# Kernel optimization log

Measured on AMD Instinct MI355X. Metric: run time of the kernel, lower is better.

Reference implementation:

```python
import jax, jax.numpy as jnp
import numpy as np

NL, D, DI, N, R, K = 32, 256, 512, 16, 16, 4   # layers, d_model, d_inner, d_state, dt_rank, d_conv
V, FF, BATCH, L = 4096, 1024, 32, 256


def _mamba_layer(x, p):
    # x: (B, L, D). One pre-norm Mamba block with residual: x + mamba(LN(x)).
    ln_w, ln_b, in_w, cw, cb, xp_w, dtw, dtb, A_log, Dskip, out_w = p
    mu = x.mean(-1, keepdims=True)
    var = ((x - mu) ** 2).mean(-1, keepdims=True)
    h = (x - mu) / jnp.sqrt(var + 1e-5) * ln_w + ln_b
    xz = jnp.einsum('bld,ed->ble', h, in_w)            # (B, L, 2*DI)
    xm, z = jnp.split(xz, 2, axis=-1)
    seq = xm.shape[1]
    # causal depthwise conv1d, kernel K, then SiLU
    xpad = jnp.pad(xm, ((0, 0), (K - 1, 0), (0, 0)))
    xc = sum(xpad[:, k:k + seq] * cw[:, k] for k in range(K)) + cb
    xc = jax.nn.silu(xc)
    dbc = jnp.einsum('ble,fe->blf', xc, xp_w)          # (B, L, R+2N)
    dt, Bm, Cm = jnp.split(dbc, [R, R + N], axis=-1)
    dt = jax.nn.softplus(jnp.einsum('blr,er->ble', dt, dtw) + dtb)  # (B, L, DI)
    A = -jnp.exp(A_log)                                # (DI, N)

    def step(hs, inp):
        dt_t, B_t, C_t, x_t = inp                      # (B,DI),(B,N),(B,N),(B,DI)
        dA = jnp.exp(dt_t[..., None] * A)              # (B, DI, N)
        hs = hs * dA + (dt_t * x_t)[..., None] * B_t[:, None, :]
        return hs, jnp.einsum('ben,bn->be', hs, C_t)

    h0 = jnp.zeros((xc.shape[0], DI, N), xc.dtype)
    _, ys = jax.lax.scan(step, h0, (dt.swapaxes(0, 1), Bm.swapaxes(0, 1), Cm.swapaxes(0, 1), xc.swapaxes(0, 1)))
    y = ys.swapaxes(0, 1) + xc * Dskip
    y = y * jax.nn.silu(z)
    return x + jnp.einsum('ble,de->bld', y, out_w)


def _stack_forward(x, params):
    return jax.lax.scan(lambda c, p: (jax.checkpoint(_mamba_layer)(c, p), None), x, params)[0]


def setup_inputs() -> dict:
    key = jax.random.key(0)
    ks = jax.random.split(key, 12)
    rn = lambda k, shape, s=0.02: jax.random.normal(k, shape, jnp.float32) * s
    return {
        'token_ids': jax.random.randint(ks[0], (BATCH, L), 0, V),
        'emb': rn(ks[1], (V, D)),
        'ln_w': jnp.ones((NL, D)), 'ln_b': jnp.zeros((NL, D)),
        'in_proj_w': rn(ks[2], (NL, 2 * DI, D)),
        'conv_w': rn(ks[3], (NL, DI, K), 0.1), 'conv_b': jnp.zeros((NL, DI)),
        'x_proj_w': rn(ks[4], (NL, R + 2 * N, DI)),
        'dt_w': rn(ks[5], (NL, DI, R), 0.1),
        'dt_b': jnp.full((NL, DI), float(np.log(np.expm1(0.01))), jnp.float32),
        'A_log': jnp.broadcast_to(jnp.log(jnp.arange(1, N + 1, dtype=jnp.float32)), (NL, DI, N)) + 0.0,
        'Dskip': jnp.ones((NL, DI)),
        'out_proj_w': rn(ks[6], (NL, D, DI)),
        'W1': rn(ks[7], (FF, D)), 'b1': jnp.zeros((FF,)),
        'W2': rn(ks[8], (V, FF)), 'b2': jnp.zeros((V,)),
    }


def reference(token_ids, emb, ln_w, ln_b, in_proj_w, conv_w, conv_b, x_proj_w, dt_w, dt_b, A_log, Dskip, out_proj_w, W1, b1, W2, b2):
    x = emb[token_ids]                                  # (B, L, D)
    params = (ln_w, ln_b, in_proj_w, conv_w, conv_b, x_proj_w, dt_w, dt_b, A_log, Dskip, out_proj_w)
    x = _stack_forward(x, params)                       # 32 stacked Mamba blocks
    h = jax.nn.relu(x @ W1.T + b1)
    return h @ W2.T + b2                                # (B, L, V) logits
```

## Files before the change

### kernel.cpp

```cpp
#include <hip/hip_runtime.h>
#include <hip/hip_bf16.h>
#include <cstdint>
#include <cstddef>


typedef __bf16 v8bf __attribute__((ext_vector_type(8)));
typedef float  v4f  __attribute__((ext_vector_type(4)));

__device__ __forceinline__ void async_copy16(const void* g, void* l) {
  __builtin_amdgcn_global_load_lds((const __attribute__((address_space(1))) void*)g,
                                   (__attribute__((address_space(3))) void*)l, 16, 0, 0);
}

__device__ __forceinline__ float bf(__bf16 v) { return (float)v; }

constexpr size_t OFF_WIN  = 0;
constexpr size_t OFF_WXP  = 16777216;
constexpr size_t OFF_WOUT = 18350080;
constexpr size_t OFF_WW1  = 26738688;
constexpr size_t OFF_WW2  = 27262976;
constexpr size_t OFF_X    = 35651584;
constexpr size_t OFF_H    = 44040192;
constexpr size_t OFF_XZ   = 48234496;
constexpr size_t OFF_DBC  = 73400320;
constexpr size_t OFF_PART = 83361792;
constexpr size_t OFF_PROD = 91750400;

__global__ __launch_bounds__(256)
void f2b_multi(const float* __restrict__ s0, const float* __restrict__ s1,
               const float* __restrict__ s2, const float* __restrict__ s3,
               const float* __restrict__ s4, char* __restrict__ ws) {
  size_t i = (size_t)blockIdx.x * 256 + threadIdx.x;
  if (i < 8388608) { ((__bf16*)(ws + OFF_WIN))[i] = (__bf16)s0[i]; return; }
  i -= 8388608;
  if (i < 786432)  { ((__bf16*)(ws + OFF_WXP))[i] = (__bf16)s1[i]; return; }
  i -= 786432;
  if (i < 4194304) { ((__bf16*)(ws + OFF_WOUT))[i] = (__bf16)s2[i]; return; }
  i -= 4194304;
  if (i < 262144)  { ((__bf16*)(ws + OFF_WW1))[i] = (__bf16)s3[i]; return; }
  i -= 262144;
  ((__bf16*)(ws + OFF_WW2))[i] = (__bf16)s4[i];
}

__global__ __launch_bounds__(256) void f2b_k(const float* __restrict__ X,
                                             __bf16* __restrict__ O) {
  size_t i = (size_t)blockIdx.x * 256 + threadIdx.x;
  O[i] = (__bf16)X[i];
}

__global__ __launch_bounds__(256)
void embed_ln_k(const int* __restrict__ tok, const float* __restrict__ emb,
                const float* __restrict__ w, const float* __restrict__ b,
                float* __restrict__ X, __bf16* __restrict__ H) {
  int row = blockIdx.x;
  int t   = threadIdx.x;
  float v = emb[(size_t)tok[row] * 256 + t];
  X[(size_t)row * 256 + t] = v;
  float s = v, q = v * v;
  #pragma unroll
  for (int o = 32; o > 0; o >>= 1) { s += __shfl_xor(s, o); q += __shfl_xor(q, o); }
  __shared__ float ss[4], qq[4];
  int wv = t >> 6;
  if ((t & 63) == 0) { ss[wv] = s; qq[wv] = q; }
  __syncthreads();
  s = ss[0] + ss[1] + ss[2] + ss[3];
  q = qq[0] + qq[1] + qq[2] + qq[3];
  float mu  = s * (1.f / 256.f);
  float var = q * (1.f / 256.f) - mu * mu;
  float r   = rsqrtf(var + 1e-5f);
  H[(size_t)row * 256 + t] = (__bf16)((v - mu) * r * w[t] + b[t]);
}

template <int EPI>
__global__ __launch_bounds__(256, 2)
void gemm_bt(const __bf16* __restrict__ A, const __bf16* __restrict__ W,
             void* outp, const float* __restrict__ bias, int M, int N, int K) {
  __shared__ __align__(16) __bf16 sA[128 * 32];
  __shared__ __align__(16) __bf16 sB[128 * 32];
  const int tid  = threadIdx.x;
  const int bm0  = blockIdx.y << 7;
  const int bn0  = blockIdx.x << 7;
  const int lane = tid & 63;
  const int wv   = tid >> 6;
  const int wm   = (wv >> 1) << 6;
  const int wn   = (wv & 1) << 6;
  const int lr   = lane & 15;
  const int lk   = lane >> 4;

  v4f acc[4][4] = {};

  const int r0 = tid >> 2;
  const int c0 = (tid & 3) << 3;
  const int wbase = (tid & ~63) << 3;

  const __bf16* gA0 = A + (size_t)(bm0 + r0) * K + c0;
  const __bf16* gA1 = A + (size_t)(bm0 + 64 + r0) * K + c0;
  const __bf16* gB0 = W + (size_t)(bn0 + r0) * K + c0;
  const __bf16* gB1 = W + (size_t)(bn0 + 64 + r0) * K + c0;

  for (int kk = 0; kk < K; kk += 32) {
    async_copy16(gA0 + kk, sA + wbase);
    async_copy16(gA1 + kk, sA + 2048 + wbase);
    async_copy16(gB0 + kk, sB + wbase);
    async_copy16(gB1 + kk, sB + 2048 + wbase);
    __syncthreads();
    v8bf af[4], bfr[4];
    #pragma unroll
    for (int i = 0; i < 4; ++i)
      af[i] = *(const v8bf*)(sA + ((wm + i * 16 + lr) << 5) + (lk << 3));
    #pragma unroll
    for (int j = 0; j < 4; ++j)
      bfr[j] = *(const v8bf*)(sB + ((wn + j * 16 + lr) << 5) + (lk << 3));
    #pragma unroll
    for (int i = 0; i < 4; ++i)
      #pragma unroll
      for (int j = 0; j < 4; ++j)
        acc[i][j] = __builtin_amdgcn_mfma_f32_16x16x32_bf16(af[i], bfr[j], acc[i][j], 0, 0, 0);
    __syncthreads();
  }

  #pragma unroll
  for (int i = 0; i < 4; ++i) {
    #pragma unroll
    for (int j = 0; j < 4; ++j) {
      int gc = bn0 + wn + j * 16 + lr;
      #pragma unroll
      for (int v = 0; v < 4; ++v) {
        int gr = bm0 + wm + i * 16 + (lk << 2) + v;
        float val = acc[i][j][v];
        size_t idx = (size_t)gr * N + gc;
        if (EPI == 0) {
          ((__bf16*)outp)[idx] = (__bf16)val;
        } else if (EPI == 1) {
          val += bias[gc]; val = fmaxf(val, 0.f);
          ((__bf16*)outp)[idx] = (__bf16)val;
        } else {
          ((float*)outp)[idx] = val + bias[gc];
        }
      }
    }
  }
}

__global__ __launch_bounds__(512, 2)
void convscan1_k(const __bf16* __restrict__ XZ,
                 const float* __restrict__ cw, const float* __restrict__ cb,
                 const __bf16* __restrict__ Wxp,
                 const float* __restrict__ dtw, const float* __restrict__ dtb,
                 const float* __restrict__ Alog,
                 float* __restrict__ DBC,
                 float* __restrict__ PART, float* __restrict__ PROD) {
  __shared__ __align__(16) __bf16 sXC[32 * 512];
  __shared__ __align__(16) float  sDBC[32 * 48];
  const int tid = threadIdx.x;
  const int c   = blockIdx.x >> 5;
  const int b   = blockIdx.x & 31;
  const int bl0 = b * 256 + c * 32;

  {
    const int r  = tid >> 4;
    const int ec = tid & 15;
    #pragma unroll
    for (int j = 0; j < 4; ++j) {
      const int e = (ec << 3) + (j << 7);
      v4f cw4[8];
      #pragma unroll
      for (int jj = 0; jj < 8; ++jj) cw4[jj] = *(const v4f*)(cw + (size_t)(e + jj) * 4);
      float a[8];
      #pragma unroll
      for (int jj = 0; jj < 8; ++jj) a[jj] = cb[e + jj];
      #pragma unroll
      for (int k = 0; k < 4; ++k) {
        if (c > 0 || r + k >= 3) {
          const v8bf xv = *(const v8bf*)(XZ + (size_t)(bl0 + r + k - 3) * 1024 + e);
          #pragma unroll
          for (int jj = 0; jj < 8; ++jj) a[jj] += bf(xv[jj]) * cw4[jj][k];
        }
      }
      v8bf outv;
      #pragma unroll
      for (int jj = 0; jj < 8; ++jj) {
        float s = a[jj] / (1.f + __expf(-a[jj]));
        outv[jj] = (__bf16)s;
      }
      const int cbk = (e >> 3) ^ (r & 7);
      *(v8bf*)(sXC + r * 512 + (cbk << 3)) = outv;
    }
  }
  __syncthreads();

  if (tid < 192) {
    const int w = tid >> 6, lane = tid & 63, lr = lane & 15, lk = lane >> 4;
    v4f acc[2] = {};
    for (int kk = 0; kk < 512; kk += 32) {
      const v8bf bfr = *(const v8bf*)(Wxp + (size_t)(w * 16 + lr) * 512 + kk + (lk << 3));
      #pragma unroll
      for (int i = 0; i < 2; ++i) {
        const int row = i * 16 + lr;
        const int cbk = (((kk >> 3) + lk) ^ (row & 7));
        const v8bf af = *(const v8bf*)(sXC + row * 512 + (cbk << 3));
        acc[i] = __builtin_amdgcn_mfma_f32_16x16x32_bf16(af, bfr, acc[i], 0, 0, 0);
      }
    }
    const int gc = w * 16 + lr;
    #pragma unroll
    for (int i = 0; i < 2; ++i)
      #pragma unroll
      for (int v = 0; v < 4; ++v)
        sDBC[(i * 16 + (lk << 2) + v) * 48 + gc] = acc[i][v];
  }
  __syncthreads();

  if (tid < 384)
    *(v4f*)(DBC + (size_t)bl0 * 48 + tid * 4) = *(const v4f*)(sDBC + tid * 4);

  if (c < 7) {
    const int e = tid;
    float Arow2[16], Wdt[16];
    #pragma unroll
    for (int n = 0; n < 16; ++n) {
      Arow2[n] = -1.4426950408889634f * __expf(Alog[(size_t)e * 16 + n]);
      Wdt[n]   = dtw[(size_t)e * 16 + n];
    }
    const float bias = dtb[e];
    float part[16], prod[16];
    #pragma unroll
    for (int n = 0; n < 16; ++n) { part[n] = 0.f; prod[n] = 1.f; }
    for (int tt = 0; tt < 32; ++tt) {
      const v4f* dp = (const v4f*)(sDBC + tt * 48);
      v4f d0 = dp[0], d1 = dp[1], d2 = dp[2], d3 = dp[3];
      v4f bv0 = dp[4], bv1 = dp[5], bv2 = dp[6], bv3 = dp[7];
      float dtv = bias;
      #pragma unroll
      for (int r = 0; r < 4; ++r)
        dtv += d0[r] * Wdt[r] + d1[r] * Wdt[r + 4] + d2[r] * Wdt[r + 8] + d3[r] * Wdt[r + 12];
      dtv = (dtv > 20.f) ? dtv : log1pf(__expf(dtv));
      const float x = bf(sXC[tt * 512 + (((e >> 3) ^ (tt & 7)) << 3) + (e & 7)]);
      const float dtx = dtv * x;
      float Bv[16];
      #pragma unroll
      for (int r = 0; r < 4; ++r) { Bv[r] = bv0[r]; Bv[r+4] = bv1[r]; Bv[r+8] = bv2[r]; Bv[r+12] = bv3[r]; }
      #pragma unroll
      for (int n = 0; n < 16; ++n) {
        const float dA = exp2f(dtv * Arow2[n]);
        part[n] = part[n] * dA + dtx * Bv[n];
        prod[n] *= dA;
      }
    }
    const size_t o = (((size_t)c * 32 + b) * 512 + e) * 16;
    #pragma unroll
    for (int rq = 0; rq < 4; ++rq) {
      v4f p, q;
      #pragma unroll
      for (int v = 0; v < 4; ++v) { p[v] = part[rq * 4 + v]; q[v] = prod[rq * 4 + v]; }
      *(v4f*)(PART + o + rq * 4) = p;
      *(v4f*)(PROD + o + rq * 4) = q;
    }
  }
}

__global__ __launch_bounds__(512, 2)
void scan2out_k(const __bf16* __restrict__ XZ,
                const float* __restrict__ cw, const float* __restrict__ cb,
                const float* __restrict__ DBC,
                const float* __restrict__ dtw, const float* __restrict__ dtb,
                const float* __restrict__ Alog, const float* __restrict__ Dskip,
                const float* __restrict__ PART, const float* __restrict__ PROD,
                const __bf16* __restrict__ Wout,
                const float* __restrict__ lnw, const float* __restrict__ lnb,
                float* __restrict__ X, __bf16* __restrict__ H) {
  __shared__ __align__(16) __bf16 sY[32 * 520];
  __shared__ __align__(16) __bf16 sB[256 * 32];
  __shared__ float sSum[4][32], sSq[4][32];
  const int tid = threadIdx.x;
  const int c   = blockIdx.x >> 5;
  const int b   = blockIdx.x & 31;
  const int bl0 = b * 256 + c * 32;
  const int e   = tid;

  float Arow2[16], Wdt[16];
  #pragma unroll
  for (int n = 0; n < 16; ++n) {
    Arow2[n] = -1.4426950408889634f * __expf(Alog[(size_t)e * 16 + n]);
    Wdt[n]   = dtw[(size_t)e * 16 + n];
  }
  const float bias = dtb[e];
  const float Dsk  = Dskip[e];
  const v4f   cwv  = *(const v4f*)(cw + (size_t)e * 4);
  const float cbe  = cb[e];

  float h[16];
  #pragma unroll
  for (int n = 0; n < 16; ++n) h[n] = 0.f;
  for (int cc = 0; cc < c; ++cc) {
    const size_t o = (((size_t)cc * 32 + b) * 512 + e) * 16;
    #pragma unroll
    for (int rq = 0; rq < 4; ++rq) {
      const v4f p = *(const v4f*)(PART + o + rq * 4);
      const v4f q = *(const v4f*)(PROD + o + rq * 4);
      #pragma unroll
      for (int v = 0; v < 4; ++v) h[rq * 4 + v] = q[v] * h[rq * 4 + v] + p[v];
    }
  }

  float w0 = 0.f, w1 = 0.f, w2 = 0.f;
  if (c > 0) {
    w0 = bf(XZ[(size_t)(bl0 - 3) * 1024 + e]);
    w1 = bf(XZ[(size_t)(bl0 - 2) * 1024 + e]);
    w2 = bf(XZ[(size_t)(bl0 - 1) * 1024 + e]);
  }

  #pragma unroll 2
  for (int tt = 0; tt < 32; ++tt) {
    const float xt = bf(XZ[(size_t)(bl0 + tt) * 1024 + e]);
    float a = cbe + w0 * cwv[0] + w1 * cwv[1] + w2 * cwv[2] + xt * cwv[3];
    const float x = a / (1.f + __expf(-a));
    w0 = w1; w1 = w2; w2 = xt;
    const float* dpf = DBC + (size_t)(bl0 + tt) * 48;
    const v4f* dp = (const v4f*)dpf;
    v4f d0 = dp[0], d1 = dp[1], d2 = dp[2], d3 = dp[3];
    v4f bv0 = dp[4], bv1 = dp[5], bv2 = dp[6], bv3 = dp[7];
    v4f cv0 = dp[8], cv1 = dp[9], cv2 = dp[10], cv3 = dp[11];
    float dtv = bias;
    #pragma unroll
    for (int r = 0; r < 4; ++r)
      dtv += d0[r] * Wdt[r] + d1[r] * Wdt[r + 4] + d2[r] * Wdt[r + 8] + d3[r] * Wdt[r + 12];
    dtv = (dtv > 20.f) ? dtv : log1pf(__expf(dtv));
    const float dtx = dtv * x;
    float Bv[16], Cv[16];
    #pragma unroll
    for (int r = 0; r < 4; ++r) {
      Bv[r] = bv0[r]; Bv[r+4] = bv1[r]; Bv[r+8] = bv2[r]; Bv[r+12] = bv3[r];
      Cv[r] = cv0[r]; Cv[r+4] = cv1[r]; Cv[r+8] = cv2[r]; Cv[r+12] = cv3[r];
    }
    float y = 0.f;
    #pragma unroll
    for (int n = 0; n < 16; ++n) {
      const float dA = exp2f(dtv * Arow2[n]);
      h[n] = h[n] * dA + dtx * Bv[n];
      y += h[n] * Cv[n];
    }
    const float z  = bf(XZ[(size_t)(bl0 + tt) * 1024 + 512 + e]);
    const float sg = z / (1.f + __expf(-z));
    sY[tt * 520 + e] = (__bf16)((y + x * Dsk) * sg);
  }
  __syncthreads();

  const int w = tid >> 6, lane = tid & 63, lr = lane & 15, lk = lane >> 4;
  const int wm = (w & 1) << 4;
  const int wn = (w >> 1) << 6;
  v4f acc[4] = {};
  for (int kk = 0; kk < 512; kk += 32) {
    async_copy16(Wout + (size_t)(tid >> 2) * 512 + ((tid & 3) << 3) + kk,
                 sB + ((tid & ~63) << 3));
    async_copy16(Wout + (size_t)(128 + (tid >> 2)) * 512 + ((tid & 3) << 3) + kk,
                 sB + 4096 + ((tid & ~63) << 3));
    __syncthreads();
    const v8bf af = *(const v8bf*)(sY + (wm + lr) * 520 + kk + (lk << 3));
    #pragma unroll
    for (int j = 0; j < 4; ++j) {
      const v8bf bfr = *(const v8bf*)(sB + ((wn + j * 16 + lr) << 5) + (lk << 3));
      acc[j] = __builtin_amdgcn_mfma_f32_16x16x32_bf16(af, bfr, acc[j], 0, 0, 0);
    }
    __syncthreads();
  }

  float s2[4], q2[4];
  #pragma unroll
  for (int v = 0; v < 4; ++v) {
    const int gr = bl0 + wm + (lk << 2) + v;
    float s = 0.f, q = 0.f;
    #pragma unroll
    for (int j = 0; j < 4; ++j) {
      const int gc = wn + j * 16 + lr;
      float val = X[(size_t)gr * 256 + gc] + acc[j][v];
      acc[j][v] = val;
      s += val; q += val * val;
    }
    #pragma unroll
    for (int o = 8; o > 0; o >>= 1) { s += __shfl_xor(s, o); q += __shfl_xor(q, o); }
    s2[v] = s; q2[v] = q;
  }
  if (lr == 0) {
    #pragma unroll
    for (int v = 0; v < 4; ++v) {
      const int row = wm + (lk << 2) + v;
      sSum[w >> 1][row] = s2[v];
      sSq[w >> 1][row]  = q2[v];
    }
  }
  __syncthreads();
  #pragma unroll
  for (int v = 0; v < 4; ++v) {
    const int row = wm + (lk << 2) + v;
    const float S = sSum[0][row] + sSum[1][row] + sSum[2][row] + sSum[3][row];
    const float Q = sSq[0][row]  + sSq[1][row]  + sSq[2][row]  + sSq[3][row];
    const float mu  = S * (1.f / 256.f);
    const float var = Q * (1.f / 256.f) - mu * mu;
    const float rinv = rsqrtf(var + 1e-5f);
    const int gr = bl0 + row;
    #pragma unroll
    for (int j = 0; j < 4; ++j) {
      const int gc = wn + j * 16 + lr;
      const float val = acc[j][v];
      X[(size_t)gr * 256 + gc] = val;
      H[(size_t)gr * 256 + gc] = (__bf16)((val - mu) * rinv * lnw[gc] + lnb[gc]);
    }
  }
}

extern "C" void kernel_launch(void* const* d_in, const int* in_sizes, int n_in,
                              void* d_out, int out_size, void* d_ws, size_t ws_size,
                              hipStream_t stream) {
  const int*   tok  = (const int*)d_in[0];
  const float* emb  = (const float*)d_in[1];
  const float* lnw  = (const float*)d_in[2];
  const float* lnb  = (const float*)d_in[3];
  const float* inw  = (const float*)d_in[4];
  const float* cw   = (const float*)d_in[5];
  const float* cb   = (const float*)d_in[6];
  const float* xpw  = (const float*)d_in[7];
  const float* dtw  = (const float*)d_in[8];
  const float* dtb  = (const float*)d_in[9];
  const float* alog = (const float*)d_in[10];
  const float* dsk  = (const float*)d_in[11];
  const float* outw = (const float*)d_in[12];
  const float* W1   = (const float*)d_in[13];
  const float* b1   = (const float*)d_in[14];
  const float* W2   = (const float*)d_in[15];
  const float* b2   = (const float*)d_in[16];

  char* ws = (char*)d_ws;
  __bf16* WIN   = (__bf16*)(ws + OFF_WIN);
  __bf16* WXP   = (__bf16*)(ws + OFF_WXP);
  __bf16* WOUT  = (__bf16*)(ws + OFF_WOUT);
  __bf16* WW1   = (__bf16*)(ws + OFF_WW1);
  __bf16* WW2   = (__bf16*)(ws + OFF_WW2);
  float*  X     = (float*)(ws + OFF_X);
  __bf16* H     = (__bf16*)(ws + OFF_H);
  __bf16* XZ    = (__bf16*)(ws + OFF_XZ);
  float*  DBC   = (float*)(ws + OFF_DBC);
  float*  PART  = (float*)(ws + OFF_PART);
  float*  PROD  = (float*)(ws + OFF_PROD);
  __bf16* XB    = (__bf16*)(ws + OFF_PART);
  __bf16* HH    = (__bf16*)(ws + OFF_PROD);

  f2b_multi<<<69632, 256, 0, stream>>>(inw, xpw, outw, W1, W2, ws);
  embed_ln_k<<<8192, 256, 0, stream>>>(tok, emb, lnw, lnb, X, H);

  for (int l = 0; l < 32; ++l) {
    const __bf16* inw_l  = WIN  + (size_t)l * 1024 * 256;
    const float*  cw_l   = cw   + (size_t)l * 512 * 4;
    const float*  cb_l   = cb   + (size_t)l * 512;
    const __bf16* xpw_l  = WXP  + (size_t)l * 48 * 512;
    const float*  dtw_l  = dtw  + (size_t)l * 512 * 16;
    const float*  dtb_l  = dtb  + (size_t)l * 512;
    const float*  alog_l = alog + (size_t)l * 512 * 16;
    const float*  dsk_l  = dsk  + (size_t)l * 512;
    const __bf16* outw_l = WOUT + (size_t)l * 256 * 512;
    const int lnx = (l + 1 < 32) ? l + 1 : 31;

    gemm_bt<0><<<dim3(8, 64), 256, 0, stream>>>(H, inw_l, XZ, nullptr, 8192, 1024, 256);
    convscan1_k<<<256, 512, 0, stream>>>(XZ, cw_l, cb_l, xpw_l, dtw_l, dtb_l,
                                         alog_l, DBC, PART, PROD);
    scan2out_k<<<256, 512, 0, stream>>>(XZ, cw_l, cb_l, DBC, dtw_l, dtb_l,
                                        alog_l, dsk_l, PART, PROD, outw_l,
                                        lnw + (size_t)lnx * 256,
                                        lnb + (size_t)lnx * 256, X, H);
  }

  f2b_k<<<8192, 256, 0, stream>>>(X, XB);
  gemm_bt<1><<<dim3(8, 64), 256, 0, stream>>>(XB, WW1, HH, b1, 8192, 1024, 256);
  gemm_bt<2><<<dim3(32, 64), 256, 0, stream>>>(HH, WW2, (float*)d_out, b2, 8192, 4096, 1024);
}
```

Before: 4.236 ms.

## Fuse next layer's in_proj GEMM into scan2out epilogue with double-buffered XZ

The next layer's input projection (LayerNorm output times W_in) now runs inside scan2out_k's epilogue, using the normalized rows staged in swizzled LDS, and writes XZ for layer l+1 into a ping-pong buffer. This removes a separate GEMM launch per layer and the round trip of H through global memory. The out_proj GEMM also drops its LDS staging of Wout and reads B fragments straight from global memory, removing two barriers per k-step. In exchange the launch bound falls to one block per CU, only 256 blocks do the in_proj work, and every block rereads the full W_in and Wout from cache.

```diff
diff --git a/kernel.cpp b/kernel.cpp
--- a/kernel.cpp
+++ b/kernel.cpp
@@ -21,10 +21,11 @@
 constexpr size_t OFF_WW2  = 27262976;
 constexpr size_t OFF_X    = 35651584;
 constexpr size_t OFF_H    = 44040192;
-constexpr size_t OFF_XZ   = 48234496;
-constexpr size_t OFF_DBC  = 73400320;
+constexpr size_t OFF_XZA  = 48234496;
+constexpr size_t OFF_XZB  = 65011712;
+constexpr size_t OFF_DBC  = 81788928;
 constexpr size_t OFF_PART = 83361792;
-constexpr size_t OFF_PROD = 91750400;
+constexpr size_t OFF_PROD = 90701824;
 
 __global__ __launch_bounds__(256)
 void f2b_multi(const float* __restrict__ s0, const float* __restrict__ s1,
@@ -259,7 +260,7 @@
   }
 }
 
-__global__ __launch_bounds__(512, 2)
+__global__ __launch_bounds__(512, 1)
 void scan2out_k(const __bf16* __restrict__ XZ,
                 const float* __restrict__ cw, const float* __restrict__ cb,
                 const float* __restrict__ DBC,
@@ -268,10 +269,11 @@
                 const float* __restrict__ PART, const float* __restrict__ PROD,
                 const __bf16* __restrict__ Wout,
                 const float* __restrict__ lnw, const float* __restrict__ lnb,
-                float* __restrict__ X, __bf16* __restrict__ H) {
+                float* __restrict__ X,
+                const __bf16* __restrict__ Wnext, __bf16* __restrict__ XZn) {
   __shared__ __align__(16) __bf16 sY[32 * 520];
-  __shared__ __align__(16) __bf16 sB[256 * 32];
   __shared__ float sSum[4][32], sSq[4][32];
+  __bf16* const sH = sY;
   const int tid = threadIdx.x;
   const int c   = blockIdx.x >> 5;
   const int b   = blockIdx.x & 31;
@@ -351,18 +353,12 @@
   const int wn = (w >> 1) << 6;
   v4f acc[4] = {};
   for (int kk = 0; kk < 512; kk += 32) {
-    async_copy16(Wout + (size_t)(tid >> 2) * 512 + ((tid & 3) << 3) + kk,
-                 sB + ((tid & ~63) << 3));
-    async_copy16(Wout + (size_t)(128 + (tid >> 2)) * 512 + ((tid & 3) << 3) + kk,
-                 sB + 4096 + ((tid & ~63) << 3));
-    __syncthreads();
     const v8bf af = *(const v8bf*)(sY + (wm + lr) * 520 + kk + (lk << 3));
     #pragma unroll
     for (int j = 0; j < 4; ++j) {
-      const v8bf bfr = *(const v8bf*)(sB + ((wn + j * 16 + lr) << 5) + (lk << 3));
+      const v8bf bfr = *(const v8bf*)(Wout + (size_t)(wn + j * 16 + lr) * 512 + kk + (lk << 3));
       acc[j] = __builtin_amdgcn_mfma_f32_16x16x32_bf16(af, bfr, acc[j], 0, 0, 0);
     }
-    __syncthreads();
   }
 
   float s2[4], q2[4];
@@ -404,8 +400,38 @@
       const int gc = wn + j * 16 + lr;
       const float val = acc[j][v];
       X[(size_t)gr * 256 + gc] = val;
-      H[(size_t)gr * 256 + gc] = (__bf16)((val - mu) * rinv * lnw[gc] + lnb[gc]);
-    }
+      if (Wnext)
+        sH[row * 256 + ((((gc >> 3)) ^ (row & 7)) << 3) + (gc & 7)] =
+            (__bf16)((val - mu) * rinv * lnw[gc] + lnb[gc]);
+    }
+  }
+
+  if (Wnext) {
+    __syncthreads();
+    const int wcol = w << 7;
+    v4f acc2[2][8] = {};
+    for (int kk = 0; kk < 256; kk += 32) {
+      const int cb16 = (kk >> 3) + lk;
+      const v8bf a0 = *(const v8bf*)(sH + lr * 256 + ((cb16 ^ (lr & 7)) << 3));
+      const v8bf a1 = *(const v8bf*)(sH + (16 + lr) * 256 + ((cb16 ^ (lr & 7)) << 3));
+      #pragma unroll
+      for (int j = 0; j < 8; ++j) {
+        const v8bf bfr = *(const v8bf*)(Wnext + (size_t)(wcol + j * 16 + lr) * 256 + kk + (lk << 3));
+        acc2[0][j] = __builtin_amdgcn_mfma_f32_16x16x32_bf16(a0, bfr, acc2[0][j], 0, 0, 0);
+        acc2[1][j] = __builtin_amdgcn_mfma_f32_16x16x32_bf16(a1, bfr, acc2[1][j], 0, 0, 0);
+      }
+    }
+    #pragma unroll
+    for (int rt = 0; rt < 2; ++rt)
+      #pragma unroll
+      for (int j = 0; j < 8; ++j) {
+        const int gc = wcol + j * 16 + lr;
+        #pragma unroll
+        for (int v = 0; v < 4; ++v) {
+          const int gr = bl0 + rt * 16 + (lk << 2) + v;
+          XZn[(size_t)gr * 1024 + gc] = (__bf16)acc2[rt][j][v];
+        }
+      }
   }
 }
 
@@ -438,18 +464,19 @@
   __bf16* WW2   = (__bf16*)(ws + OFF_WW2);
   float*  X     = (float*)(ws + OFF_X);
   __bf16* H     = (__bf16*)(ws + OFF_H);
-  __bf16* XZ    = (__bf16*)(ws + OFF_XZ);
+  __bf16* XZA   = (__bf16*)(ws + OFF_XZA);
+  __bf16* XZB   = (__bf16*)(ws + OFF_XZB);
   float*  DBC   = (float*)(ws + OFF_DBC);
   float*  PART  = (float*)(ws + OFF_PART);
   float*  PROD  = (float*)(ws + OFF_PROD);
-  __bf16* XB    = (__bf16*)(ws + OFF_PART);
-  __bf16* HH    = (__bf16*)(ws + OFF_PROD);
+  __bf16* XB    = (__bf16*)(ws + OFF_XZA);
+  __bf16* HH    = (__bf16*)(ws + OFF_XZB);
 
   f2b_multi<<<69632, 256, 0, stream>>>(inw, xpw, outw, W1, W2, ws);
   embed_ln_k<<<8192, 256, 0, stream>>>(tok, emb, lnw, lnb, X, H);
+  gemm_bt<0><<<dim3(8, 64), 256, 0, stream>>>(H, WIN, XZA, nullptr, 8192, 1024, 256);
 
   for (int l = 0; l < 32; ++l) {
-    const __bf16* inw_l  = WIN  + (size_t)l * 1024 * 256;
     const float*  cw_l   = cw   + (size_t)l * 512 * 4;
     const float*  cb_l   = cb   + (size_t)l * 512;
     const __bf16* xpw_l  = WXP  + (size_t)l * 48 * 512;
@@ -459,14 +486,17 @@
     const float*  dsk_l  = dsk  + (size_t)l * 512;
     const __bf16* outw_l = WOUT + (size_t)l * 256 * 512;
     const int lnx = (l + 1 < 32) ? l + 1 : 31;
-
-    gemm_bt<0><<<dim3(8, 64), 256, 0, stream>>>(H, inw_l, XZ, nullptr, 8192, 1024, 256);
-    convscan1_k<<<256, 512, 0, stream>>>(XZ, cw_l, cb_l, xpw_l, dtw_l, dtb_l,
+    __bf16* XZ_in  = (l & 1) ? XZB : XZA;
+    __bf16* XZ_out = (l & 1) ? XZA : XZB;
+    const __bf16* wnext = (l + 1 < 32) ? WIN + (size_t)(l + 1) * 1024 * 256 : nullptr;
+
+    convscan1_k<<<256, 512, 0, stream>>>(XZ_in, cw_l, cb_l, xpw_l, dtw_l, dtb_l,
                                          alog_l, DBC, PART, PROD);
-    scan2out_k<<<256, 512, 0, stream>>>(XZ, cw_l, cb_l, DBC, dtw_l, dtb_l,
+    scan2out_k<<<256, 512, 0, stream>>>(XZ_in, cw_l, cb_l, DBC, dtw_l, dtb_l,
                                         alog_l, dsk_l, PART, PROD, outw_l,
                                         lnw + (size_t)lnx * 256,
-                                        lnb + (size_t)lnx * 256, X, H);
+                                        lnb + (size_t)lnx * 256, X,
+                                        wnext, XZ_out);
   }
 
   f2b_k<<<8192, 256, 0, stream>>>(X, XB);
```

Measured after the change: 4.620 ms. +9.1%, slower.

## Halve scan chunk size, replace stored decay products with dt sums, precompute A

Applied to the files above, without the earlier changes.

The chunked selective scan now uses 16-timestep chunks instead of 32. This doubles the block count of the conv/scan and scan/out-proj kernels to 512 and raises their launch-bounds occupancy hint. The per-chunk decay product array is no longer stored; each chunk stores only the sum of dt, and the carry-in decay is recomputed as exp2(A*sum), which cuts the PROD traffic. -exp(A_log)*log2e is computed once in the weight-conversion prologue instead of in every block. The cost is a longer serial prefix over more chunks in the second kernel, and the out-projection tile per block shrinks to 16 rows.

```diff
diff --git a/kernel.cpp b/kernel.cpp
--- a/kernel.cpp
+++ b/kernel.cpp
@@ -22,14 +22,16 @@
 constexpr size_t OFF_X    = 35651584;
 constexpr size_t OFF_H    = 44040192;
 constexpr size_t OFF_XZ   = 48234496;
-constexpr size_t OFF_DBC  = 73400320;
-constexpr size_t OFF_PART = 83361792;
-constexpr size_t OFF_PROD = 91750400;
+constexpr size_t OFF_DBC  = 65011712;
+constexpr size_t OFF_PART = 66584576;
+constexpr size_t OFF_SS   = 82313216;
+constexpr size_t OFF_A2   = 83296256;
 
 __global__ __launch_bounds__(256)
 void f2b_multi(const float* __restrict__ s0, const float* __restrict__ s1,
                const float* __restrict__ s2, const float* __restrict__ s3,
-               const float* __restrict__ s4, char* __restrict__ ws) {
+               const float* __restrict__ s4, const float* __restrict__ s5,
+               char* __restrict__ ws) {
   size_t i = (size_t)blockIdx.x * 256 + threadIdx.x;
   if (i < 8388608) { ((__bf16*)(ws + OFF_WIN))[i] = (__bf16)s0[i]; return; }
   i -= 8388608;
@@ -39,7 +41,9 @@
   i -= 4194304;
   if (i < 262144)  { ((__bf16*)(ws + OFF_WW1))[i] = (__bf16)s3[i]; return; }
   i -= 262144;
-  ((__bf16*)(ws + OFF_WW2))[i] = (__bf16)s4[i];
+  if (i < 4194304) { ((__bf16*)(ws + OFF_WW2))[i] = (__bf16)s4[i]; return; }
+  i -= 4194304;
+  ((float*)(ws + OFF_A2))[i] = -1.4426950408889634f * __expf(s5[i]);
 }
 
 __global__ __launch_bounds__(256) void f2b_k(const float* __restrict__ X,
@@ -142,27 +146,27 @@
   }
 }
 
-__global__ __launch_bounds__(512, 2)
+__global__ __launch_bounds__(512, 4)
 void convscan1_k(const __bf16* __restrict__ XZ,
                  const float* __restrict__ cw, const float* __restrict__ cb,
                  const __bf16* __restrict__ Wxp,
                  const float* __restrict__ dtw, const float* __restrict__ dtb,
-                 const float* __restrict__ Alog,
+                 const float* __restrict__ A2,
                  float* __restrict__ DBC,
-                 float* __restrict__ PART, float* __restrict__ PROD) {
-  __shared__ __align__(16) __bf16 sXC[32 * 512];
-  __shared__ __align__(16) float  sDBC[32 * 48];
+                 float* __restrict__ PART, float* __restrict__ SS) {
+  __shared__ __align__(16) __bf16 sXC[16 * 512];
+  __shared__ __align__(16) float  sDBC[16 * 48];
   const int tid = threadIdx.x;
   const int c   = blockIdx.x >> 5;
   const int b   = blockIdx.x & 31;
-  const int bl0 = b * 256 + c * 32;
+  const int bl0 = b * 256 + c * 16;
 
   {
-    const int r  = tid >> 4;
-    const int ec = tid & 15;
-    #pragma unroll
-    for (int j = 0; j < 4; ++j) {
-      const int e = (ec << 3) + (j << 7);
+    const int r  = tid >> 5;
+    const int ec = tid & 31;
+    #pragma unroll
+    for (int j = 0; j < 2; ++j) {
+      const int e = (ec << 3) + (j << 8);
       v4f cw4[8];
       #pragma unroll
       for (int jj = 0; jj < 8; ++jj) cw4[jj] = *(const v4f*)(cw + (size_t)(e + jj) * 4);
@@ -191,98 +195,96 @@
 
   if (tid < 192) {
     const int w = tid >> 6, lane = tid & 63, lr = lane & 15, lk = lane >> 4;
-    v4f acc[2] = {};
+    v4f acc = {};
     for (int kk = 0; kk < 512; kk += 32) {
       const v8bf bfr = *(const v8bf*)(Wxp + (size_t)(w * 16 + lr) * 512 + kk + (lk << 3));
-      #pragma unroll
-      for (int i = 0; i < 2; ++i) {
-        const int row = i * 16 + lr;
-        const int cbk = (((kk >> 3) + lk) ^ (row & 7));
-        const v8bf af = *(const v8bf*)(sXC + row * 512 + (cbk << 3));
-        acc[i] = __builtin_amdgcn_mfma_f32_16x16x32_bf16(af, bfr, acc[i], 0, 0, 0);
-      }
+      const int cbk = (((kk >> 3) + lk) ^ (lr & 7));
+      const v8bf af = *(const v8bf*)(sXC + lr * 512 + (cbk << 3));
+      acc = __builtin_amdgcn_mfma_f32_16x16x32_bf16(af, bfr, acc, 0, 0, 0);
     }
     const int gc = w * 16 + lr;
     #pragma unroll
-    for (int i = 0; i < 2; ++i)
-      #pragma unroll
-      for (int v = 0; v < 4; ++v)
-        sDBC[(i * 16 + (lk << 2) + v) * 48 + gc] = acc[i][v];
+    for (int v = 0; v < 4; ++v)
+      sDBC[((lk << 2) + v) * 48 + gc] = acc[v];
   }
   __syncthreads();
 
-  if (tid < 384)
+  if (tid < 192)
     *(v4f*)(DBC + (size_t)bl0 * 48 + tid * 4) = *(const v4f*)(sDBC + tid * 4);
 
-  if (c < 7) {
+  if (c < 15) {
     const int e = tid;
-    float Arow2[16], Wdt[16];
-    #pragma unroll
-    for (int n = 0; n < 16; ++n) {
-      Arow2[n] = -1.4426950408889634f * __expf(Alog[(size_t)e * 16 + n]);
-      Wdt[n]   = dtw[(size_t)e * 16 + n];
+    v4f a2[4], wd[4];
+    #pragma unroll
+    for (int q = 0; q < 4; ++q) {
+      a2[q] = *(const v4f*)(A2  + (size_t)e * 16 + q * 4);
+      wd[q] = *(const v4f*)(dtw + (size_t)e * 16 + q * 4);
     }
     const float bias = dtb[e];
-    float part[16], prod[16];
-    #pragma unroll
-    for (int n = 0; n < 16; ++n) { part[n] = 0.f; prod[n] = 1.f; }
-    for (int tt = 0; tt < 32; ++tt) {
+    float part[16];
+    #pragma unroll
+    for (int n = 0; n < 16; ++n) part[n] = 0.f;
+    float S = 0.f;
+    for (int tt = 0; tt < 16; ++tt) {
       const v4f* dp = (const v4f*)(sDBC + tt * 48);
-      v4f d0 = dp[0], d1 = dp[1], d2 = dp[2], d3 = dp[3];
-      v4f bv0 = dp[4], bv1 = dp[5], bv2 = dp[6], bv3 = dp[7];
       float dtv = bias;
-      #pragma unroll
-      for (int r = 0; r < 4; ++r)
-        dtv += d0[r] * Wdt[r] + d1[r] * Wdt[r + 4] + d2[r] * Wdt[r + 8] + d3[r] * Wdt[r + 12];
+      {
+        const v4f d0 = dp[0], d1 = dp[1], d2 = dp[2], d3 = dp[3];
+        #pragma unroll
+        for (int r = 0; r < 4; ++r)
+          dtv += d0[r] * wd[0][r] + d1[r] * wd[1][r] + d2[r] * wd[2][r] + d3[r] * wd[3][r];
+      }
       dtv = (dtv > 20.f) ? dtv : log1pf(__expf(dtv));
       const float x = bf(sXC[tt * 512 + (((e >> 3) ^ (tt & 7)) << 3) + (e & 7)]);
       const float dtx = dtv * x;
-      float Bv[16];
-      #pragma unroll
-      for (int r = 0; r < 4; ++r) { Bv[r] = bv0[r]; Bv[r+4] = bv1[r]; Bv[r+8] = bv2[r]; Bv[r+12] = bv3[r]; }
-      #pragma unroll
-      for (int n = 0; n < 16; ++n) {
-        const float dA = exp2f(dtv * Arow2[n]);
-        part[n] = part[n] * dA + dtx * Bv[n];
-        prod[n] *= dA;
+      S += dtv;
+      {
+        const v4f bv0 = dp[4], bv1 = dp[5], bv2 = dp[6], bv3 = dp[7];
+        #pragma unroll
+        for (int v = 0; v < 4; ++v) {
+          part[v]      = part[v]      * exp2f(dtv * a2[0][v]) + dtx * bv0[v];
+          part[4 + v]  = part[4 + v]  * exp2f(dtv * a2[1][v]) + dtx * bv1[v];
+          part[8 + v]  = part[8 + v]  * exp2f(dtv * a2[2][v]) + dtx * bv2[v];
+          part[12 + v] = part[12 + v] * exp2f(dtv * a2[3][v]) + dtx * bv3[v];
+        }
       }
     }
     const size_t o = (((size_t)c * 32 + b) * 512 + e) * 16;
     #pragma unroll
     for (int rq = 0; rq < 4; ++rq) {
-      v4f p, q;
-      #pragma unroll
-      for (int v = 0; v < 4; ++v) { p[v] = part[rq * 4 + v]; q[v] = prod[rq * 4 + v]; }
+      v4f p;
+      #pragma unroll
+      for (int v = 0; v < 4; ++v) p[v] = part[rq * 4 + v];
       *(v4f*)(PART + o + rq * 4) = p;
-      *(v4f*)(PROD + o + rq * 4) = q;
-    }
-  }
-}
-
-__global__ __launch_bounds__(512, 2)
+    }
+    SS[((size_t)c * 32 + b) * 512 + e] = S;
+  }
+}
+
+__global__ __launch_bounds__(512, 4)
 void scan2out_k(const __bf16* __restrict__ XZ,
                 const float* __restrict__ cw, const float* __restrict__ cb,
                 const float* __restrict__ DBC,
                 const float* __restrict__ dtw, const float* __restrict__ dtb,
-                const float* __restrict__ Alog, const float* __restrict__ Dskip,
-                const float* __restrict__ PART, const float* __restrict__ PROD,
+                const float* __restrict__ A2, const float* __restrict__ Dskip,
+                const float* __restrict__ PART, const float* __restrict__ SS,
                 const __bf16* __restrict__ Wout,
                 const float* __restrict__ lnw, const float* __restrict__ lnb,
                 float* __restrict__ X, __bf16* __restrict__ H) {
-  __shared__ __align__(16) __bf16 sY[32 * 520];
+  __shared__ __align__(16) __bf16 sY[16 * 520];
   __shared__ __align__(16) __bf16 sB[256 * 32];
-  __shared__ float sSum[4][32], sSq[4][32];
+  __shared__ float sSum[8][16], sSq[8][16];
   const int tid = threadIdx.x;
   const int c   = blockIdx.x >> 5;
   const int b   = blockIdx.x & 31;
-  const int bl0 = b * 256 + c * 32;
+  const int bl0 = b * 256 + c * 16;
   const int e   = tid;
 
-  float Arow2[16], Wdt[16];
-  #pragma unroll
-  for (int n = 0; n < 16; ++n) {
-    Arow2[n] = -1.4426950408889634f * __expf(Alog[(size_t)e * 16 + n]);
-    Wdt[n]   = dtw[(size_t)e * 16 + n];
+  v4f a2[4], wd[4];
+  #pragma unroll
+  for (int q = 0; q < 4; ++q) {
+    a2[q] = *(const v4f*)(A2  + (size_t)e * 16 + q * 4);
+    wd[q] = *(const v4f*)(dtw + (size_t)e * 16 + q * 4);
   }
   const float bias = dtb[e];
   const float Dsk  = Dskip[e];
@@ -293,13 +295,14 @@
   #pragma unroll
   for (int n = 0; n < 16; ++n) h[n] = 0.f;
   for (int cc = 0; cc < c; ++cc) {
+    const float S  = SS[((size_t)cc * 32 + b) * 512 + e];
     const size_t o = (((size_t)cc * 32 + b) * 512 + e) * 16;
     #pragma unroll
     for (int rq = 0; rq < 4; ++rq) {
       const v4f p = *(const v4f*)(PART + o + rq * 4);
-      const v4f q = *(const v4f*)(PROD + o + rq * 4);
-      #pragma unroll
-      for (int v = 0; v < 4; ++v) h[rq * 4 + v] = q[v] * h[rq * 4 + v] + p[v];
+      #pragma unroll
+      for (int v = 0; v < 4; ++v)
+        h[rq * 4 + v] = h[rq * 4 + v] * exp2f(a2[rq][v] * S) + p[v];
     }
   }
 
@@ -310,35 +313,32 @@
     w2 = bf(XZ[(size_t)(bl0 - 1) * 1024 + e]);
   }
 
-  #pragma unroll 2
-  for (int tt = 0; tt < 32; ++tt) {
+  for (int tt = 0; tt < 16; ++tt) {
     const float xt = bf(XZ[(size_t)(bl0 + tt) * 1024 + e]);
     float a = cbe + w0 * cwv[0] + w1 * cwv[1] + w2 * cwv[2] + xt * cwv[3];
     const float x = a / (1.f + __expf(-a));
     w0 = w1; w1 = w2; w2 = xt;
-    const float* dpf = DBC + (size_t)(bl0 + tt) * 48;
-    const v4f* dp = (const v4f*)dpf;
-    v4f d0 = dp[0], d1 = dp[1], d2 = dp[2], d3 = dp[3];
-    v4f bv0 = dp[4], bv1 = dp[5], bv2 = dp[6], bv3 = dp[7];
-    v4f cv0 = dp[8], cv1 = dp[9], cv2 = dp[10], cv3 = dp[11];
+    const v4f* dp = (const v4f*)(DBC + (size_t)(bl0 + tt) * 48);
     float dtv = bias;
-    #pragma unroll
-    for (int r = 0; r < 4; ++r)
-      dtv += d0[r] * Wdt[r] + d1[r] * Wdt[r + 4] + d2[r] * Wdt[r + 8] + d3[r] * Wdt[r + 12];
+    {
+      const v4f d0 = dp[0], d1 = dp[1], d2 = dp[2], d3 = dp[3];
+      #pragma unroll
+      for (int r = 0; r < 4; ++r)
+        dtv += d0[r] * wd[0][r] + d1[r] * wd[1][r] + d2[r] * wd[2][r] + d3[r] * wd[3][r];
+    }
     dtv = (dtv > 20.f) ? dtv : log1pf(__expf(dtv));
     const float dtx = dtv * x;
-    float Bv[16], Cv[16];
-    #pragma unroll
-    for (int r = 0; r < 4; ++r) {
-      Bv[r] = bv0[r]; Bv[r+4] = bv1[r]; Bv[r+8] = bv2[r]; Bv[r+12] = bv3[r];
-      Cv[r] = cv0[r]; Cv[r+4] = cv1[r]; Cv[r+8] = cv2[r]; Cv[r+12] = cv3[r];
-    }
     float y = 0.f;
-    #pragma unroll
-    for (int n = 0; n < 16; ++n) {
-      const float dA = exp2f(dtv * Arow2[n]);
-      h[n] = h[n] * dA + dtx * Bv[n];
-      y += h[n] * Cv[n];
+    {
+      const v4f bv0 = dp[4], bv1 = dp[5], bv2 = dp[6], bv3 = dp[7];
+      const v4f cv0 = dp[8], cv1 = dp[9], cv2 = dp[10], cv3 = dp[11];
+      #pragma unroll
+      for (int v = 0; v < 4; ++v) {
+        h[v]      = h[v]      * exp2f(dtv * a2[0][v]) + dtx * bv0[v];  y += h[v]      * cv0[v];
+        h[4 + v]  = h[4 + v]  * exp2f(dtv * a2[1][v]) + dtx * bv1[v];  y += h[4 + v]  * cv1[v];
+        h[8 + v]  = h[8 + v]  * exp2f(dtv * a2[2][v]) + dtx * bv2[v];  y += h[8 + v]  * cv2[v];
+        h[12 + v] = h[12 + v] * exp2f(dtv * a2[3][v]) + dtx * bv3[v];  y += h[12 + v] * cv3[v];
+      }
     }
     const float z  = bf(XZ[(size_t)(bl0 + tt) * 1024 + 512 + e]);
     const float sg = z / (1.f + __expf(-z));
@@ -347,18 +347,17 @@
   __syncthreads();
 
   const int w = tid >> 6, lane = tid & 63, lr = lane & 15, lk = lane >> 4;
-  const int wm = (w & 1) << 4;
-  const int wn = (w >> 1) << 6;
-  v4f acc[4] = {};
+  const int wn = w << 5;
+  v4f acc[2] = {};
   for (int kk = 0; kk < 512; kk += 32) {
     async_copy16(Wout + (size_t)(tid >> 2) * 512 + ((tid & 3) << 3) + kk,
                  sB + ((tid & ~63) << 3));
     async_copy16(Wout + (size_t)(128 + (tid >> 2)) * 512 + ((tid & 3) << 3) + kk,
                  sB + 4096 + ((tid & ~63) << 3));
     __syncthreads();
-    const v8bf af = *(const v8bf*)(sY + (wm + lr) * 520 + kk + (lk << 3));
-    #pragma unroll
-    for (int j = 0; j < 4; ++j) {
+    const v8bf af = *(const v8bf*)(sY + lr * 520 + kk + (lk << 3));
+    #pragma unroll
+    for (int j = 0; j < 2; ++j) {
       const v8bf bfr = *(const v8bf*)(sB + ((wn + j * 16 + lr) << 5) + (lk << 3));
       acc[j] = __builtin_amdgcn_mfma_f32_16x16x32_bf16(af, bfr, acc[j], 0, 0, 0);
     }
@@ -368,10 +367,10 @@
   float s2[4], q2[4];
   #pragma unroll
   for (int v = 0; v < 4; ++v) {
-    const int gr = bl0 + wm + (lk << 2) + v;
+    const int gr = bl0 + (lk << 2) + v;
     float s = 0.f, q = 0.f;
     #pragma unroll
-    for (int j = 0; j < 4; ++j) {
+    for (int j = 0; j < 2; ++j) {
       const int gc = wn + j * 16 + lr;
       float val = X[(size_t)gr * 256 + gc] + acc[j][v];
       acc[j][v] = val;
@@ -384,23 +383,24 @@
   if (lr == 0) {
     #pragma unroll
     for (int v = 0; v < 4; ++v) {
-      const int row = wm + (lk << 2) + v;
-      sSum[w >> 1][row] = s2[v];
-      sSq[w >> 1][row]  = q2[v];
+      const int row = (lk << 2) + v;
+      sSum[w][row] = s2[v];
+      sSq[w][row]  = q2[v];
     }
   }
   __syncthreads();
   #pragma unroll
   for (int v = 0; v < 4; ++v) {
-    const int row = wm + (lk << 2) + v;
-    const float S = sSum[0][row] + sSum[1][row] + sSum[2][row] + sSum[3][row];
-    const float Q = sSq[0][row]  + sSq[1][row]  + sSq[2][row]  + sSq[3][row];
-    const float mu  = S * (1.f / 256.f);
-    const float var = Q * (1.f / 256.f) - mu * mu;
+    const int row = (lk << 2) + v;
+    float S = 0.f, Q = 0.f;
+    #pragma unroll
+    for (int ww = 0; ww < 8; ++ww) { S += sSum[ww][row]; Q += sSq[ww][row]; }
+    const float mu   = S * (1.f / 256.f);
+    const float var  = Q * (1.f / 256.f) - mu * mu;
     const float rinv = rsqrtf(var + 1e-5f);
     const int gr = bl0 + row;
     #pragma unroll
-    for (int j = 0; j < 4; ++j) {
+    for (int j = 0; j < 2; ++j) {
       const int gc = wn + j * 16 + lr;
       const float val = acc[j][v];
       X[(size_t)gr * 256 + gc] = val;
@@ -441,30 +441,31 @@
   __bf16* XZ    = (__bf16*)(ws + OFF_XZ);
   float*  DBC   = (float*)(ws + OFF_DBC);
   float*  PART  = (float*)(ws + OFF_PART);
-  float*  PROD  = (float*)(ws + OFF_PROD);
+  float*  SS    = (float*)(ws + OFF_SS);
+  float*  A2    = (float*)(ws + OFF_A2);
   __bf16* XB    = (__bf16*)(ws + OFF_PART);
-  __bf16* HH    = (__bf16*)(ws + OFF_PROD);
-
-  f2b_multi<<<69632, 256, 0, stream>>>(inw, xpw, outw, W1, W2, ws);
+  __bf16* HH    = (__bf16*)(ws + OFF_PART + 8388608);
+
+  f2b_multi<<<70656, 256, 0, stream>>>(inw, xpw, outw, W1, W2, alog, ws);
   embed_ln_k<<<8192, 256, 0, stream>>>(tok, emb, lnw, lnb, X, H);
 
   for (int l = 0; l < 32; ++l) {
-    const __bf16* inw_l  = WIN  + (size_t)l * 1024 * 256;
     const float*  cw_l   = cw   + (size_t)l * 512 * 4;
     const float*  cb_l   = cb   + (size_t)l * 512;
     const __bf16* xpw_l  = WXP  + (size_t)l * 48 * 512;
     const float*  dtw_l  = dtw  + (size_t)l * 512 * 16;
     const float*  dtb_l  = dtb  + (size_t)l * 512;
-    const float*  alog_l = alog + (size_t)l * 512 * 16;
+    const float*  A2_l   = A2   + (size_t)l * 512 * 16;
     const float*  dsk_l  = dsk  + (size_t)l * 512;
+    const __bf16* inw_l  = WIN  + (size_t)l * 1024 * 256;
     const __bf16* outw_l = WOUT + (size_t)l * 256 * 512;
     const int lnx = (l + 1 < 32) ? l + 1 : 31;
 
     gemm_bt<0><<<dim3(8, 64), 256, 0, stream>>>(H, inw_l, XZ, nullptr, 8192, 1024, 256);
-    convscan1_k<<<256, 512, 0, stream>>>(XZ, cw_l, cb_l, xpw_l, dtw_l, dtb_l,
-                                         alog_l, DBC, PART, PROD);
-    scan2out_k<<<256, 512, 0, stream>>>(XZ, cw_l, cb_l, DBC, dtw_l, dtb_l,
-                                        alog_l, dsk_l, PART, PROD, outw_l,
+    convscan1_k<<<512, 512, 0, stream>>>(XZ, cw_l, cb_l, xpw_l, dtw_l, dtb_l,
+                                         A2_l, DBC, PART, SS);
+    scan2out_k<<<512, 512, 0, stream>>>(XZ, cw_l, cb_l, DBC, dtw_l, dtb_l,
+                                        A2_l, dsk_l, PART, SS, outw_l,
                                         lnw + (size_t)lnx * 256,
                                         lnb + (size_t)lnx * 256, X, H);
   }
```

Result: no change. 4.244 ms (+0.2%).
